# Performance work log

Measured on AMD Instinct MI355X. Metric: run time of the kernel, lower is better.

The kernel has to match this reference:

```python
import jax, jax.numpy as jnp
import numpy as np

N = 50000      # nodes
E = 600000     # edges (avg degree 12)
D = 128        # input_dim == hidden_dim (required: same Linear reused across pool layers)
OUT = 64       # output_dim
NUM_POOL = 2   # num_pool_layers


def setup_inputs() -> dict:
    key = jax.random.key(0)
    ks = jax.random.split(key, 8)
    s = 1.0 / np.sqrt(D)  # fan-in style scaling keeps repeated scatter-adds stable
    x = jax.random.normal(ks[0], (N, D), dtype=jnp.float32)
    edge_index = jax.random.randint(ks[1], (2, E), 0, N, dtype=jnp.int64)
    W1 = jax.random.normal(ks[2], (D, D), dtype=jnp.float32) * s
    b1 = jnp.zeros((D,), dtype=jnp.float32)
    W2 = jax.random.normal(ks[3], (D, D), dtype=jnp.float32) * s
    b2 = jnp.zeros((D,), dtype=jnp.float32)
    Wout = jax.random.normal(ks[4], (D, OUT), dtype=jnp.float32) * s
    bout = jnp.zeros((OUT,), dtype=jnp.float32)
    return {"x": x, "edge_index": edge_index, "W1": W1, "b1": b1,
            "W2": W2, "b2": b2, "Wout": Wout, "bout": bout}


def _gauss_seidel_pool(x, W, b, src, dst, num_layers):
    # PyG MessagePassing(aggr='add'): out[i] = sum_{edges (j->i)} lin(x[j]).
    # Nodes with no incoming edges become zero (propagate replaces x entirely).
    for _ in range(num_layers):
        m = x @ W + b                      # [N, out] linear once per node (== lin(x_j) per edge)
        x = jax.ops.segment_sum(m[src], dst, num_segments=N)  # gather + scatter-add
    return x


def reference(x, edge_index, W1, b1, W2, b2, Wout, bout):
    src = edge_index[0]  # x_j source
    dst = edge_index[1]  # aggregation target i
    h = _gauss_seidel_pool(x, W1, b1, src, dst, NUM_POOL)
    h = jax.nn.relu(h)                     # dropout = identity (eval mode)
    h = _gauss_seidel_pool(h, W2, b2, src, dst, NUM_POOL)
    h = jax.nn.relu(h)
    return h @ Wout + bout                 # [N, OUT]
```

## Files before the change

kernel.cpp:

```cpp
#include <hip/hip_runtime.h>


static inline int ceil_div(int a, int b) { return (a + b - 1) / b; }

typedef __attribute__((ext_vector_type(8))) short bf16x8;
typedef __attribute__((ext_vector_type(4))) float f32x4;

__device__ inline unsigned short f2bf(float f) {
    unsigned u = __float_as_uint(f);
    return (unsigned short)((u + 0x7fffu + ((u >> 16) & 1u)) >> 16);
}


__device__ void wprep_dev(const float* __restrict__ W, unsigned short* __restrict__ hi,
                          int total, int C, int g0, int G) {
    for (int t = g0; t < total; t += G) {
        int j = t & 7;
        int lane = (t >> 3) & 63;
        int f = t >> 9;
        int c = f & 3, ct = f >> 2;
        int k = c * 32 + (lane >> 4) * 8 + j;
        int col = ct * 16 + (lane & 15);
        hi[t] = f2bf(W[(size_t)k * C + col]);
    }
}

__global__ __launch_bounds__(256) void prep_kernel(const float* __restrict__ W1,
                                                   const float* __restrict__ W2,
                                                   const float* __restrict__ Wout,
                                                   unsigned short* __restrict__ W1hi,
                                                   unsigned short* __restrict__ W2hi,
                                                   unsigned short* __restrict__ Wohi,
                                                   int* __restrict__ cursor,
                                                   unsigned* __restrict__ stat,
                                                   int N, int nChunks) {
    int g0 = blockIdx.x * 256 + threadIdx.x;
    int G = gridDim.x * 256;
    for (int i = g0; i < N; i += G) cursor[i] = 0;
    for (int i = g0; i < nChunks; i += G) stat[i] = 0;
    wprep_dev(W1, W1hi, 128 * 128, 128, g0, G);
    wprep_dev(W2, W2hi, 128 * 128, 128, g0, G);
    wprep_dev(Wout, Wohi, 128 * 64, 64, g0, G);
}


__global__ __launch_bounds__(256) void hist_kernel(const int* __restrict__ dst,
                                                   int* __restrict__ deg, int E) {
    int e = blockIdx.x * 256 + threadIdx.x;
    if (e < E) atomicAdd(&deg[dst[e]], 1);
}

__global__ __launch_bounds__(256) void scan_fuse_kernel(const int* __restrict__ deg,
                                                        int* __restrict__ rp,
                                                        int* __restrict__ cursor,
                                                        unsigned* __restrict__ stat,
                                                        int N) {
    __shared__ int s[256];
    int c = blockIdx.x, tid = threadIdx.x;
    int i = c * 256 + tid;
    int v = (i < N) ? deg[i] : 0;
    s[tid] = v;
    __syncthreads();
    for (int off = 1; off < 256; off <<= 1) {
        int t = (tid >= off) ? s[tid - off] : 0;
        __syncthreads();
        s[tid] += t;
        __syncthreads();
    }
    int loc = s[tid] - v;
    int tot = s[255];
    __syncthreads();
    if (tid == 0) atomicExch(&stat[c], (unsigned)tot | 0x80000000u);

    unsigned mine = 0;
    if (tid < c) {
        unsigned u;
        do { u = atomicAdd(&stat[tid], 0u); } while (!(u & 0x80000000u));
        mine = u & 0x7fffffffu;
    }
    s[tid] = (int)mine;
    __syncthreads();
    for (int off = 128; off >= 1; off >>= 1) {
        if (tid < off) s[tid] += s[tid + off];
        __syncthreads();
    }
    int prefix = s[0];
    if (i <= N) {
        int val = loc + prefix;
        rp[i] = val;
        if (i < N) cursor[i] = val;
    }
}

__global__ __launch_bounds__(256) void fill_kernel(const int* __restrict__ src,
                                                   const int* __restrict__ dst,
                                                   int* __restrict__ cursor,
                                                   unsigned short* __restrict__ es, int E) {
    int e = blockIdx.x * 256 + threadIdx.x;
    if (e < E) {
        int p = atomicAdd(&cursor[dst[e]], 1);
        es[p] = (unsigned short)src[e];
    }
}


__global__ __launch_bounds__(256) void gemm1_kernel(const float* __restrict__ X,
                                                    const uint4* __restrict__ Whi,
                                                    const float* __restrict__ Bias,
                                                    unsigned short* __restrict__ Y, int n) {
    int tid = threadIdx.x;
    int wave = tid >> 6, lane = tid & 63;
    int lm = lane & 15, lq = lane >> 4;
    int r0 = blockIdx.x * 64;

    bf16x8 afr[4][4];
#pragma unroll
    for (int rt = 0; rt < 4; ++rt) {
        int ar = r0 + rt * 16 + lm;
        if (ar > n - 1) ar = n - 1;
#pragma unroll
        for (int c = 0; c < 4; ++c) {
            int k = c * 32 + lq * 8;
            const float* ap = X + (size_t)ar * 128 + k;
            float4 f0 = ((const float4*)ap)[0];
            float4 f1 = ((const float4*)ap)[1];
            bf16x8 v;
            v[0] = (short)f2bf(f0.x); v[1] = (short)f2bf(f0.y);
            v[2] = (short)f2bf(f0.z); v[3] = (short)f2bf(f0.w);
            v[4] = (short)f2bf(f1.x); v[5] = (short)f2bf(f1.y);
            v[6] = (short)f2bf(f1.z); v[7] = (short)f2bf(f1.w);
            afr[rt][c] = v;
        }
    }

    f32x4 acc[4][2];
#pragma unroll
    for (int rt = 0; rt < 4; ++rt)
#pragma unroll
        for (int t = 0; t < 2; ++t)
            acc[rt][t] = (f32x4){0.f, 0.f, 0.f, 0.f};

#pragma unroll
    for (int c = 0; c < 4; ++c) {
#pragma unroll
        for (int t = 0; t < 2; ++t) {
            int ct = wave * 2 + t;
            uint4 uh = Whi[(ct * 4 + c) * 64 + lane];
            bf16x8 wh = *(const bf16x8*)&uh;
#pragma unroll
            for (int rt = 0; rt < 4; ++rt)
                acc[rt][t] = __builtin_amdgcn_mfma_f32_16x16x32_bf16(afr[rt][c], wh, acc[rt][t], 0, 0, 0);
        }
    }

#pragma unroll
    for (int t = 0; t < 2; ++t) {
        int col = (wave * 2 + t) * 16 + lm;
        float bias = Bias[col];
#pragma unroll
        for (int rt = 0; rt < 4; ++rt) {
#pragma unroll
            for (int r = 0; r < 4; ++r) {
                int row = r0 + rt * 16 + lq * 4 + r;
                if (row < n)
                    Y[(size_t)row * 128 + col] = f2bf(acc[rt][t][r] + bias);
            }
        }
    }
}


__device__ inline void acc_row8(float* a, uint4 v) {
    a[0] += __uint_as_float(v.x << 16);
    a[1] += __uint_as_float(v.x & 0xffff0000u);
    a[2] += __uint_as_float(v.y << 16);
    a[3] += __uint_as_float(v.y & 0xffff0000u);
    a[4] += __uint_as_float(v.z << 16);
    a[5] += __uint_as_float(v.z & 0xffff0000u);
    a[6] += __uint_as_float(v.w << 16);
    a[7] += __uint_as_float(v.w & 0xffff0000u);
}

template <int COLS, bool OUTF32>
__global__ __launch_bounds__(256) void fused_agg_gemm_kernel(const unsigned short* __restrict__ M,
                                                             const int* __restrict__ rp,
                                                             const unsigned short* __restrict__ es,
                                                             const uint4* __restrict__ Whi,
                                                             const float* __restrict__ Bias,
                                                             void* __restrict__ Yv,
                                                             int n, int do_relu) {
    constexpr int CT_W = COLS / 64;
    constexpr int SR = 136;
    __shared__ unsigned short Hl[32 * SR];

    int tid = threadIdx.x;
    int r0 = blockIdx.x * 32;

    {
        int sub = tid >> 4, ln = tid & 15;
#pragma unroll 1
        for (int q = 0; q < 2; ++q) {
            int nl = sub * 2 + q;
            int node = r0 + nl;
            float acc[8] = {};
            if (node < n) {
                int beg = rp[node], end = rp[node + 1];
                int e = beg;
                for (; e + 8 <= end; e += 8) {
                    int s0 = es[e],     s1 = es[e + 1], s2 = es[e + 2], s3 = es[e + 3];
                    int s4 = es[e + 4], s5 = es[e + 5], s6 = es[e + 6], s7 = es[e + 7];
                    uint4 v0 = ((const uint4*)(M + (size_t)s0 * 128))[ln];
                    uint4 v1 = ((const uint4*)(M + (size_t)s1 * 128))[ln];
                    uint4 v2 = ((const uint4*)(M + (size_t)s2 * 128))[ln];
                    uint4 v3 = ((const uint4*)(M + (size_t)s3 * 128))[ln];
                    uint4 v4 = ((const uint4*)(M + (size_t)s4 * 128))[ln];
                    uint4 v5 = ((const uint4*)(M + (size_t)s5 * 128))[ln];
                    uint4 v6 = ((const uint4*)(M + (size_t)s6 * 128))[ln];
                    uint4 v7 = ((const uint4*)(M + (size_t)s7 * 128))[ln];
                    acc_row8(acc, v0); acc_row8(acc, v1);
                    acc_row8(acc, v2); acc_row8(acc, v3);
                    acc_row8(acc, v4); acc_row8(acc, v5);
                    acc_row8(acc, v6); acc_row8(acc, v7);
                }
                for (; e + 4 <= end; e += 4) {
                    int s0 = es[e], s1 = es[e + 1], s2 = es[e + 2], s3 = es[e + 3];
                    uint4 v0 = ((const uint4*)(M + (size_t)s0 * 128))[ln];
                    uint4 v1 = ((const uint4*)(M + (size_t)s1 * 128))[ln];
                    uint4 v2 = ((const uint4*)(M + (size_t)s2 * 128))[ln];
                    uint4 v3 = ((const uint4*)(M + (size_t)s3 * 128))[ln];
                    acc_row8(acc, v0); acc_row8(acc, v1);
                    acc_row8(acc, v2); acc_row8(acc, v3);
                }
                for (; e < end; ++e) {
                    uint4 v = ((const uint4*)(M + (size_t)es[e] * 128))[ln];
                    acc_row8(acc, v);
                }
                if (do_relu) {
#pragma unroll
                    for (int i = 0; i < 8; ++i) acc[i] = fmaxf(acc[i], 0.f);
                }
            }
            uint4 o;
            o.x = (unsigned)f2bf(acc[0]) | ((unsigned)f2bf(acc[1]) << 16);
            o.y = (unsigned)f2bf(acc[2]) | ((unsigned)f2bf(acc[3]) << 16);
            o.z = (unsigned)f2bf(acc[4]) | ((unsigned)f2bf(acc[5]) << 16);
            o.w = (unsigned)f2bf(acc[6]) | ((unsigned)f2bf(acc[7]) << 16);
            *(uint4*)(&Hl[nl * SR + ln * 8]) = o;
        }
    }
    __syncthreads();

    int wave = tid >> 6, lane = tid & 63;
    int lm = lane & 15, lq = lane >> 4;

    f32x4 acc[2][CT_W];
#pragma unroll
    for (int rt = 0; rt < 2; ++rt)
#pragma unroll
        for (int t = 0; t < CT_W; ++t)
            acc[rt][t] = (f32x4){0.f, 0.f, 0.f, 0.f};

#pragma unroll
    for (int c = 0; c < 4; ++c) {
        bf16x8 afr[2];
#pragma unroll
        for (int rt = 0; rt < 2; ++rt)
            afr[rt] = *(const bf16x8*)(&Hl[(rt * 16 + lm) * SR + c * 32 + lq * 8]);
#pragma unroll
        for (int t = 0; t < CT_W; ++t) {
            int ct = wave * CT_W + t;
            uint4 uh = Whi[(ct * 4 + c) * 64 + lane];
            bf16x8 wh = *(const bf16x8*)&uh;
#pragma unroll
            for (int rt = 0; rt < 2; ++rt)
                acc[rt][t] = __builtin_amdgcn_mfma_f32_16x16x32_bf16(afr[rt], wh, acc[rt][t], 0, 0, 0);
        }
    }

#pragma unroll
    for (int t = 0; t < CT_W; ++t) {
        int col = (wave * CT_W + t) * 16 + lm;
        float bias = Bias[col];
#pragma unroll
        for (int rt = 0; rt < 2; ++rt) {
#pragma unroll
            for (int r = 0; r < 4; ++r) {
                int row = r0 + rt * 16 + lq * 4 + r;
                if (row < n) {
                    float v = acc[rt][t][r] + bias;
                    if (OUTF32)
                        ((float*)Yv)[(size_t)row * COLS + col] = v;
                    else
                        ((unsigned short*)Yv)[(size_t)row * COLS + col] = f2bf(v);
                }
            }
        }
    }
}


extern "C" void kernel_launch(void* const* d_in, const int* in_sizes, int n_in,
                              void* d_out, int out_size, void* d_ws, size_t ws_size,
                              hipStream_t stream) {
    const float* x    = (const float*)d_in[0];
    const int*   ei   = (const int*)d_in[1];
    const float* W1   = (const float*)d_in[2];
    const float* b1   = (const float*)d_in[3];
    const float* W2   = (const float*)d_in[4];
    const float* b2   = (const float*)d_in[5];
    const float* Wout = (const float*)d_in[6];
    const float* bout = (const float*)d_in[7];
    float*       out  = (float*)d_out;

    const int N = in_sizes[0] / 128;
    const int E = in_sizes[1] / 2;
    const int* src = ei;
    const int* dst = ei + E;

    char* ws = (char*)d_ws;
    auto take = [&](size_t bytes) {
        char* p = ws;
        ws += (bytes + 255) & ~(size_t)255;
        return p;
    };
    unsigned short* mA = (unsigned short*)take((size_t)N * 128 * 2);
    unsigned short* mB = (unsigned short*)take((size_t)N * 128 * 2);
    unsigned short* W1hi = (unsigned short*)take(128 * 128 * 2);
    unsigned short* W2hi = (unsigned short*)take(128 * 128 * 2);
    unsigned short* Wohi = (unsigned short*)take(128 * 64 * 2);
    int* rp      = (int*)take((size_t)(N + 1) * sizeof(int));
    int* cursor  = (int*)take((size_t)N * sizeof(int));
    unsigned short* es = (unsigned short*)take((size_t)E * sizeof(unsigned short));
    unsigned* stat = (unsigned*)take(4096);

    const int nChunks = ceil_div(N + 1, 256);
    const int tiles64 = ceil_div(N, 64);
    const int tiles32 = ceil_div(N, 32);

    prep_kernel<<<256, 256, 0, stream>>>(W1, W2, Wout, W1hi, W2hi, Wohi,
                                         cursor, stat, N, nChunks);
    hist_kernel<<<ceil_div(E, 256), 256, 0, stream>>>(dst, cursor, E);
    scan_fuse_kernel<<<nChunks, 256, 0, stream>>>(cursor, rp, cursor, stat, N);
    fill_kernel<<<ceil_div(E, 256), 256, 0, stream>>>(src, dst, cursor, es, E);
    gemm1_kernel<<<tiles64, 256, 0, stream>>>(x, (const uint4*)W1hi, b1, mA, N);

    fused_agg_gemm_kernel<128, false><<<tiles32, 256, 0, stream>>>(
        mA, rp, es, (const uint4*)W1hi, b1, mB, N, 0);
    fused_agg_gemm_kernel<128, false><<<tiles32, 256, 0, stream>>>(
        mB, rp, es, (const uint4*)W2hi, b2, mA, N, 1);
    fused_agg_gemm_kernel<128, false><<<tiles32, 256, 0, stream>>>(
        mA, rp, es, (const uint4*)W2hi, b2, mB, N, 0);
    fused_agg_gemm_kernel<64, true><<<tiles32, 256, 0, stream>>>(
        mB, rp, es, (const uint4*)Wohi, bout, out, N, 1);
}
```

Before: 299.7 us.

## Balance edge aggregation across block via edge-chunk partitioning and LDS atomics

Each block now covers 64 nodes. Instead of assigning fixed nodes per thread group, the block's contiguous CSR edge range is split into 8-edge chunks spread over 16 groups. Each chunk finds its starting node by binary search over a shared row-pointer copy and flushes partial sums into an fp32 shared accumulator with atomicAdd. This is meant to remove load imbalance from varying degrees and to keep eight gathers in flight. ReLU and bf16 conversion move into the MFMA operand load, and the GEMM uses four row tiles per wave. The cost is LDS atomics, a larger shared footprint (about 33 KB, which may lower occupancy), and half as many blocks.

```diff
diff --git a/kernel.cpp b/kernel.cpp
--- a/kernel.cpp
+++ b/kernel.cpp
@@ -190,62 +190,66 @@
                                                              void* __restrict__ Yv,
                                                              int n, int do_relu) {
     constexpr int CT_W = COLS / 64;
-    constexpr int SR = 136;
-    __shared__ unsigned short Hl[32 * SR];
+    constexpr int SRF = 132;
+    __shared__ float sAcc[64 * SRF];
+    __shared__ int rpl[65];
 
     int tid = threadIdx.x;
-    int r0 = blockIdx.x * 32;
+    int r0 = blockIdx.x * 64;
+
+    if (tid < 65) {
+        int gi = r0 + tid;
+        if (gi > n) gi = n;
+        rpl[tid] = rp[gi];
+    }
+    for (int i = tid; i < 64 * SRF / 4; i += 256)
+        ((float4*)sAcc)[i] = make_float4(0.f, 0.f, 0.f, 0.f);
+    __syncthreads();
 
     {
-        int sub = tid >> 4, ln = tid & 15;
+        int g = tid >> 4, ln = tid & 15;
+        int beg = rpl[0], end = rpl[64];
+        int nc = (end - beg + 7) >> 3;
 #pragma unroll 1
-        for (int q = 0; q < 2; ++q) {
-            int nl = sub * 2 + q;
-            int node = r0 + nl;
+        for (int c = g; c < nc; c += 16) {
+            int e0 = beg + (c << 3);
+            int cnt = end - e0;
+            if (cnt > 8) cnt = 8;
+
+            int sidx[8];
+#pragma unroll
+            for (int j = 0; j < 8; ++j) sidx[j] = (j < cnt) ? (int)es[e0 + j] : 0;
+            uint4 rows[8];
+#pragma unroll
+            for (int j = 0; j < 8; ++j)
+                if (j < cnt) rows[j] = ((const uint4*)(M + (size_t)sidx[j] * 128))[ln];
+
+            int lo = 0, hi = 64;
+#pragma unroll
+            for (int it = 0; it < 6; ++it) {
+                int mid = (lo + hi) >> 1;
+                if (rpl[mid] <= e0) lo = mid; else hi = mid;
+            }
+            int nl = lo;
+
             float acc[8] = {};
-            if (node < n) {
-                int beg = rp[node], end = rp[node + 1];
-                int e = beg;
-                for (; e + 8 <= end; e += 8) {
-                    int s0 = es[e],     s1 = es[e + 1], s2 = es[e + 2], s3 = es[e + 3];
-                    int s4 = es[e + 4], s5 = es[e + 5], s6 = es[e + 6], s7 = es[e + 7];
-                    uint4 v0 = ((const uint4*)(M + (size_t)s0 * 128))[ln];
-                    uint4 v1 = ((const uint4*)(M + (size_t)s1 * 128))[ln];
-                    uint4 v2 = ((const uint4*)(M + (size_t)s2 * 128))[ln];
-                    uint4 v3 = ((const uint4*)(M + (size_t)s3 * 128))[ln];
-                    uint4 v4 = ((const uint4*)(M + (size_t)s4 * 128))[ln];
-                    uint4 v5 = ((const uint4*)(M + (size_t)s5 * 128))[ln];
-                    uint4 v6 = ((const uint4*)(M + (size_t)s6 * 128))[ln];
-                    uint4 v7 = ((const uint4*)(M + (size_t)s7 * 128))[ln];
-                    acc_row8(acc, v0); acc_row8(acc, v1);
-                    acc_row8(acc, v2); acc_row8(acc, v3);
-                    acc_row8(acc, v4); acc_row8(acc, v5);
-                    acc_row8(acc, v6); acc_row8(acc, v7);
+#pragma unroll
+            for (int j = 0; j < 8; ++j) {
+                if (j >= cnt) break;
+                int e = e0 + j;
+                if (e >= rpl[nl + 1]) {
+#pragma unroll
+                    for (int k = 0; k < 8; ++k)
+                        atomicAdd(&sAcc[nl * SRF + ln * 8 + k], acc[k]);
+#pragma unroll
+                    for (int k = 0; k < 8; ++k) acc[k] = 0.f;
+                    do { ++nl; } while (e >= rpl[nl + 1]);
                 }
-                for (; e + 4 <= end; e += 4) {
-                    int s0 = es[e], s1 = es[e + 1], s2 = es[e + 2], s3 = es[e + 3];
-                    uint4 v0 = ((const uint4*)(M + (size_t)s0 * 128))[ln];
-                    uint4 v1 = ((const uint4*)(M + (size_t)s1 * 128))[ln];
-                    uint4 v2 = ((const uint4*)(M + (size_t)s2 * 128))[ln];
-                    uint4 v3 = ((const uint4*)(M + (size_t)s3 * 128))[ln];
-                    acc_row8(acc, v0); acc_row8(acc, v1);
-                    acc_row8(acc, v2); acc_row8(acc, v3);
-                }
-                for (; e < end; ++e) {
-                    uint4 v = ((const uint4*)(M + (size_t)es[e] * 128))[ln];
-                    acc_row8(acc, v);
-                }
-                if (do_relu) {
-#pragma unroll
-                    for (int i = 0; i < 8; ++i) acc[i] = fmaxf(acc[i], 0.f);
-                }
-            }
-            uint4 o;
-            o.x = (unsigned)f2bf(acc[0]) | ((unsigned)f2bf(acc[1]) << 16);
-            o.y = (unsigned)f2bf(acc[2]) | ((unsigned)f2bf(acc[3]) << 16);
-            o.z = (unsigned)f2bf(acc[4]) | ((unsigned)f2bf(acc[5]) << 16);
-            o.w = (unsigned)f2bf(acc[6]) | ((unsigned)f2bf(acc[7]) << 16);
-            *(uint4*)(&Hl[nl * SR + ln * 8]) = o;
+                acc_row8(acc, rows[j]);
+            }
+#pragma unroll
+            for (int k = 0; k < 8; ++k)
+                atomicAdd(&sAcc[nl * SRF + ln * 8 + k], acc[k]);
         }
     }
     __syncthreads();
@@ -253,26 +257,41 @@
     int wave = tid >> 6, lane = tid & 63;
     int lm = lane & 15, lq = lane >> 4;
 
-    f32x4 acc[2][CT_W];
-#pragma unroll
-    for (int rt = 0; rt < 2; ++rt)
+    f32x4 acc[4][CT_W];
+#pragma unroll
+    for (int rt = 0; rt < 4; ++rt)
 #pragma unroll
         for (int t = 0; t < CT_W; ++t)
             acc[rt][t] = (f32x4){0.f, 0.f, 0.f, 0.f};
 
 #pragma unroll
     for (int c = 0; c < 4; ++c) {
-        bf16x8 afr[2];
-#pragma unroll
-        for (int rt = 0; rt < 2; ++rt)
-            afr[rt] = *(const bf16x8*)(&Hl[(rt * 16 + lm) * SR + c * 32 + lq * 8]);
+        bf16x8 afr[4];
+#pragma unroll
+        for (int rt = 0; rt < 4; ++rt) {
+            const float* ap = &sAcc[(rt * 16 + lm) * SRF + c * 32 + lq * 8];
+            float4 a0 = ((const float4*)ap)[0];
+            float4 a1 = ((const float4*)ap)[1];
+            if (do_relu) {
+                a0.x = fmaxf(a0.x, 0.f); a0.y = fmaxf(a0.y, 0.f);
+                a0.z = fmaxf(a0.z, 0.f); a0.w = fmaxf(a0.w, 0.f);
+                a1.x = fmaxf(a1.x, 0.f); a1.y = fmaxf(a1.y, 0.f);
+                a1.z = fmaxf(a1.z, 0.f); a1.w = fmaxf(a1.w, 0.f);
+            }
+            bf16x8 v;
+            v[0] = (short)f2bf(a0.x); v[1] = (short)f2bf(a0.y);
+            v[2] = (short)f2bf(a0.z); v[3] = (short)f2bf(a0.w);
+            v[4] = (short)f2bf(a1.x); v[5] = (short)f2bf(a1.y);
+            v[6] = (short)f2bf(a1.z); v[7] = (short)f2bf(a1.w);
+            afr[rt] = v;
+        }
 #pragma unroll
         for (int t = 0; t < CT_W; ++t) {
             int ct = wave * CT_W + t;
             uint4 uh = Whi[(ct * 4 + c) * 64 + lane];
             bf16x8 wh = *(const bf16x8*)&uh;
 #pragma unroll
-            for (int rt = 0; rt < 2; ++rt)
+            for (int rt = 0; rt < 4; ++rt)
                 acc[rt][t] = __builtin_amdgcn_mfma_f32_16x16x32_bf16(afr[rt], wh, acc[rt][t], 0, 0, 0);
         }
     }
@@ -282,7 +301,7 @@
         int col = (wave * CT_W + t) * 16 + lm;
         float bias = Bias[col];
 #pragma unroll
-        for (int rt = 0; rt < 2; ++rt) {
+        for (int rt = 0; rt < 4; ++rt) {
 #pragma unroll
             for (int r = 0; r < 4; ++r) {
                 int row = r0 + rt * 16 + lq * 4 + r;
@@ -335,7 +354,6 @@
 
     const int nChunks = ceil_div(N + 1, 256);
     const int tiles64 = ceil_div(N, 64);
-    const int tiles32 = ceil_div(N, 32);
 
     prep_kernel<<<256, 256, 0, stream>>>(W1, W2, Wout, W1hi, W2hi, Wohi,
                                          cursor, stat, N, nChunks);
@@ -344,12 +362,12 @@
     fill_kernel<<<ceil_div(E, 256), 256, 0, stream>>>(src, dst, cursor, es, E);
     gemm1_kernel<<<tiles64, 256, 0, stream>>>(x, (const uint4*)W1hi, b1, mA, N);
 
-    fused_agg_gemm_kernel<128, false><<<tiles32, 256, 0, stream>>>(
+    fused_agg_gemm_kernel<128, false><<<tiles64, 256, 0, stream>>>(
         mA, rp, es, (const uint4*)W1hi, b1, mB, N, 0);
-    fused_agg_gemm_kernel<128, false><<<tiles32, 256, 0, stream>>>(
+    fused_agg_gemm_kernel<128, false><<<tiles64, 256, 0, stream>>>(
         mB, rp, es, (const uint4*)W2hi, b2, mA, N, 1);
-    fused_agg_gemm_kernel<128, false><<<tiles32, 256, 0, stream>>>(
+    fused_agg_gemm_kernel<128, false><<<tiles64, 256, 0, stream>>>(
         mA, rp, es, (const uint4*)W2hi, b2, mB, N, 0);
-    fused_agg_gemm_kernel<64, true><<<tiles32, 256, 0, stream>>>(
+    fused_agg_gemm_kernel<64, true><<<tiles64, 256, 0, stream>>>(
         mB, rp, es, (const uint4*)Wohi, bout, out, N, 1);
 }
```

New measurement: 650.6 us. 117% more time.

## Degree-sort nodes within 64-row tiles to balance gather work across lanes

Applied to the files above, without the earlier changes.

Each block of the fused aggregate+GEMM kernel now handles 64 nodes instead of 32. It loads the row pointers into shared memory and ranks nodes by in-degree, so the 16-lane groups process nodes in descending-degree order over four rounds. This is meant to reduce divergence and tail imbalance between groups, and to amortize weight-fragment loads over more MFMA row tiles. In exchange the block needs more shared memory and accumulator registers, adds an O(64) ranking pass with extra barriers, and launches half as many blocks.

```diff
diff --git a/kernel.cpp b/kernel.cpp
--- a/kernel.cpp
+++ b/kernel.cpp
@@ -191,54 +191,71 @@
                                                              int n, int do_relu) {
     constexpr int CT_W = COLS / 64;
     constexpr int SR = 136;
-    __shared__ unsigned short Hl[32 * SR];
+    __shared__ unsigned short Hl[64 * SR];
+    __shared__ int rpl[65];
+    __shared__ unsigned char perm[64];
 
     int tid = threadIdx.x;
-    int r0 = blockIdx.x * 32;
+    int r0 = blockIdx.x * 64;
+
+    if (tid < 65) {
+        int gi = r0 + tid;
+        if (gi > n) gi = n;
+        rpl[tid] = rp[gi];
+    }
+    __syncthreads();
+
+    if (tid < 64) {
+        int di = rpl[tid + 1] - rpl[tid];
+        int rank = 0;
+        for (int j = 0; j < 64; ++j) {
+            int dj = rpl[j + 1] - rpl[j];
+            rank += (dj > di) || (dj == di && j < tid);
+        }
+        perm[rank] = (unsigned char)tid;
+    }
+    __syncthreads();
 
     {
-        int sub = tid >> 4, ln = tid & 15;
+        int g = tid >> 4, ln = tid & 15;
 #pragma unroll 1
-        for (int q = 0; q < 2; ++q) {
-            int nl = sub * 2 + q;
-            int node = r0 + nl;
+        for (int q = 0; q < 4; ++q) {
+            int nl = perm[q * 16 + g];
+            int beg = rpl[nl], end = rpl[nl + 1];
             float acc[8] = {};
-            if (node < n) {
-                int beg = rp[node], end = rp[node + 1];
-                int e = beg;
-                for (; e + 8 <= end; e += 8) {
-                    int s0 = es[e],     s1 = es[e + 1], s2 = es[e + 2], s3 = es[e + 3];
-                    int s4 = es[e + 4], s5 = es[e + 5], s6 = es[e + 6], s7 = es[e + 7];
-                    uint4 v0 = ((const uint4*)(M + (size_t)s0 * 128))[ln];
-                    uint4 v1 = ((const uint4*)(M + (size_t)s1 * 128))[ln];
-                    uint4 v2 = ((const uint4*)(M + (size_t)s2 * 128))[ln];
-                    uint4 v3 = ((const uint4*)(M + (size_t)s3 * 128))[ln];
-                    uint4 v4 = ((const uint4*)(M + (size_t)s4 * 128))[ln];
-                    uint4 v5 = ((const uint4*)(M + (size_t)s5 * 128))[ln];
-                    uint4 v6 = ((const uint4*)(M + (size_t)s6 * 128))[ln];
-                    uint4 v7 = ((const uint4*)(M + (size_t)s7 * 128))[ln];
-                    acc_row8(acc, v0); acc_row8(acc, v1);
-                    acc_row8(acc, v2); acc_row8(acc, v3);
-                    acc_row8(acc, v4); acc_row8(acc, v5);
-                    acc_row8(acc, v6); acc_row8(acc, v7);
-                }
-                for (; e + 4 <= end; e += 4) {
-                    int s0 = es[e], s1 = es[e + 1], s2 = es[e + 2], s3 = es[e + 3];
-                    uint4 v0 = ((const uint4*)(M + (size_t)s0 * 128))[ln];
-                    uint4 v1 = ((const uint4*)(M + (size_t)s1 * 128))[ln];
-                    uint4 v2 = ((const uint4*)(M + (size_t)s2 * 128))[ln];
-                    uint4 v3 = ((const uint4*)(M + (size_t)s3 * 128))[ln];
-                    acc_row8(acc, v0); acc_row8(acc, v1);
-                    acc_row8(acc, v2); acc_row8(acc, v3);
-                }
-                for (; e < end; ++e) {
-                    uint4 v = ((const uint4*)(M + (size_t)es[e] * 128))[ln];
-                    acc_row8(acc, v);
-                }
-                if (do_relu) {
-#pragma unroll
-                    for (int i = 0; i < 8; ++i) acc[i] = fmaxf(acc[i], 0.f);
-                }
+            int e = beg;
+            for (; e + 8 <= end; e += 8) {
+                int s0 = es[e],     s1 = es[e + 1], s2 = es[e + 2], s3 = es[e + 3];
+                int s4 = es[e + 4], s5 = es[e + 5], s6 = es[e + 6], s7 = es[e + 7];
+                uint4 v0 = ((const uint4*)(M + (size_t)s0 * 128))[ln];
+                uint4 v1 = ((const uint4*)(M + (size_t)s1 * 128))[ln];
+                uint4 v2 = ((const uint4*)(M + (size_t)s2 * 128))[ln];
+                uint4 v3 = ((const uint4*)(M + (size_t)s3 * 128))[ln];
+                uint4 v4 = ((const uint4*)(M + (size_t)s4 * 128))[ln];
+                uint4 v5 = ((const uint4*)(M + (size_t)s5 * 128))[ln];
+                uint4 v6 = ((const uint4*)(M + (size_t)s6 * 128))[ln];
+                uint4 v7 = ((const uint4*)(M + (size_t)s7 * 128))[ln];
+                acc_row8(acc, v0); acc_row8(acc, v1);
+                acc_row8(acc, v2); acc_row8(acc, v3);
+                acc_row8(acc, v4); acc_row8(acc, v5);
+                acc_row8(acc, v6); acc_row8(acc, v7);
+            }
+            for (; e + 4 <= end; e += 4) {
+                int s0 = es[e], s1 = es[e + 1], s2 = es[e + 2], s3 = es[e + 3];
+                uint4 v0 = ((const uint4*)(M + (size_t)s0 * 128))[ln];
+                uint4 v1 = ((const uint4*)(M + (size_t)s1 * 128))[ln];
+                uint4 v2 = ((const uint4*)(M + (size_t)s2 * 128))[ln];
+                uint4 v3 = ((const uint4*)(M + (size_t)s3 * 128))[ln];
+                acc_row8(acc, v0); acc_row8(acc, v1);
+                acc_row8(acc, v2); acc_row8(acc, v3);
+            }
+            for (; e < end; ++e) {
+                uint4 v = ((const uint4*)(M + (size_t)es[e] * 128))[ln];
+                acc_row8(acc, v);
+            }
+            if (do_relu) {
+#pragma unroll
+                for (int i = 0; i < 8; ++i) acc[i] = fmaxf(acc[i], 0.f);
             }
             uint4 o;
             o.x = (unsigned)f2bf(acc[0]) | ((unsigned)f2bf(acc[1]) << 16);
@@ -253,18 +270,18 @@
     int wave = tid >> 6, lane = tid & 63;
     int lm = lane & 15, lq = lane >> 4;
 
-    f32x4 acc[2][CT_W];
-#pragma unroll
-    for (int rt = 0; rt < 2; ++rt)
+    f32x4 acc[4][CT_W];
+#pragma unroll
+    for (int rt = 0; rt < 4; ++rt)
 #pragma unroll
         for (int t = 0; t < CT_W; ++t)
             acc[rt][t] = (f32x4){0.f, 0.f, 0.f, 0.f};
 
 #pragma unroll
     for (int c = 0; c < 4; ++c) {
-        bf16x8 afr[2];
-#pragma unroll
-        for (int rt = 0; rt < 2; ++rt)
+        bf16x8 afr[4];
+#pragma unroll
+        for (int rt = 0; rt < 4; ++rt)
             afr[rt] = *(const bf16x8*)(&Hl[(rt * 16 + lm) * SR + c * 32 + lq * 8]);
 #pragma unroll
         for (int t = 0; t < CT_W; ++t) {
@@ -272,7 +289,7 @@
             uint4 uh = Whi[(ct * 4 + c) * 64 + lane];
             bf16x8 wh = *(const bf16x8*)&uh;
 #pragma unroll
-            for (int rt = 0; rt < 2; ++rt)
+            for (int rt = 0; rt < 4; ++rt)
                 acc[rt][t] = __builtin_amdgcn_mfma_f32_16x16x32_bf16(afr[rt], wh, acc[rt][t], 0, 0, 0);
         }
     }
@@ -282,7 +299,7 @@
         int col = (wave * CT_W + t) * 16 + lm;
         float bias = Bias[col];
 #pragma unroll
-        for (int rt = 0; rt < 2; ++rt) {
+        for (int rt = 0; rt < 4; ++rt) {
 #pragma unroll
             for (int r = 0; r < 4; ++r) {
                 int row = r0 + rt * 16 + lq * 4 + r;
@@ -335,7 +352,6 @@
 
     const int nChunks = ceil_div(N + 1, 256);
     const int tiles64 = ceil_div(N, 64);
-    const int tiles32 = ceil_div(N, 32);
 
     prep_kernel<<<256, 256, 0, stream>>>(W1, W2, Wout, W1hi, W2hi, Wohi,
                                          cursor, stat, N, nChunks);
@@ -344,12 +360,12 @@
     fill_kernel<<<ceil_div(E, 256), 256, 0, stream>>>(src, dst, cursor, es, E);
     gemm1_kernel<<<tiles64, 256, 0, stream>>>(x, (const uint4*)W1hi, b1, mA, N);
 
-    fused_agg_gemm_kernel<128, false><<<tiles32, 256, 0, stream>>>(
+    fused_agg_gemm_kernel<128, false><<<tiles64, 256, 0, stream>>>(
         mA, rp, es, (const uint4*)W1hi, b1, mB, N, 0);
-    fused_agg_gemm_kernel<128, false><<<tiles32, 256, 0, stream>>>(
+    fused_agg_gemm_kernel<128, false><<<tiles64, 256, 0, stream>>>(
         mB, rp, es, (const uint4*)W2hi, b2, mA, N, 1);
-    fused_agg_gemm_kernel<128, false><<<tiles32, 256, 0, stream>>>(
+    fused_agg_gemm_kernel<128, false><<<tiles64, 256, 0, stream>>>(
         mA, rp, es, (const uint4*)W2hi, b2, mB, N, 0);
-    fused_agg_gemm_kernel<64, true><<<tiles32, 256, 0, stream>>>(
+    fused_agg_gemm_kernel<64, true><<<tiles64, 256, 0, stream>>>(
         mB, rp, es, (const uint4*)Wohi, bout, out, N, 1);
 }
```

Result: faster. 288.1 us (-3.9%).
